# Kernel optimization log

Measured on AMD Instinct MI355X. Metric: run time of the kernel, lower is better.

Reference implementation:

```python
import jax, jax.numpy as jnp
import numpy as np

# einspline cubic B-spline basis matrix (4x4)
BASIS = jnp.array([[-1.0, 3.0, -3.0, 1.0],
                   [ 3.0, -6.0, 0.0, 4.0],
                   [-3.0, 3.0, 3.0, 1.0],
                   [ 1.0, 0.0, 0.0, 0.0]], dtype=jnp.float32) / 6.0


def _build_1d_system_matrix(M: int) -> jnp.ndarray:
    """(M+2, M+2) natural-boundary interpolating B-spline system matrix."""
    delta = 1.0 / (M - 1)
    dinv2 = (1.0 / delta) ** 2
    A = np.zeros((M + 2, M + 2), dtype=np.float32)
    A[0, 0] = dinv2; A[0, 1] = -2.0 * dinv2; A[0, 2] = dinv2
    i = np.arange(1, M + 1)
    A[i, i - 1] = 1.0 / 6.0
    A[i, i] = 2.0 / 3.0
    A[i, i + 1] = 1.0 / 6.0
    A[M + 1, M - 1] = dinv2; A[M + 1, M] = -2.0 * dinv2; A[M + 1, M + 1] = dinv2
    return jnp.asarray(A)


def find_coefs_2d(data: jnp.ndarray) -> jnp.ndarray:
    """data: (C, Mx, My) -> coefs: (C, Mx+2, My+2) via separable solves."""
    C, Mx, My = data.shape
    Ax = _build_1d_system_matrix(Mx)
    Ay = _build_1d_system_matrix(My)
    # solve along x for every (c, y)
    d = jnp.transpose(data, (0, 2, 1)).reshape(-1, Mx)          # (C*My, Mx)
    Bx = jnp.zeros((d.shape[0], Mx + 2), dtype=data.dtype).at[:, 1:Mx + 1].set(d)
    cx = jnp.linalg.solve(Ax, Bx.T).T                           # (C*My, Mx+2)
    cx = jnp.transpose(cx.reshape(C, My, Mx + 2), (0, 2, 1))    # (C, Mx+2, My)
    # solve along y for every (c, x)
    d2 = cx.reshape(-1, My)                                      # (C*(Mx+2), My)
    By = jnp.zeros((d2.shape[0], My + 2), dtype=data.dtype).at[:, 1:My + 1].set(d2)
    coefs = jnp.linalg.solve(Ay, By.T).T.reshape(C, Mx + 2, My + 2)
    return coefs


def _axis_index(un: jnp.ndarray, M: int):
    """Cell index + local fraction with out-of-range extrapolation handling."""
    i = jnp.floor(un).astype(jnp.int32)
    t = un - i.astype(un.dtype)
    low = un < 0
    i = jnp.where(low, 0, i)
    t = jnp.where(low, un, t)
    high = un >= M - 2
    i = jnp.where(high, M - 2, i)
    t = jnp.where(high, un - (M - 2), t)
    return i, t


def interpolate_grid_2d(coefs: jnp.ndarray, u: jnp.ndarray) -> jnp.ndarray:
    """coefs: (C, Mx+2, My+2); u: (B, 2) in [0,1]^2 -> (B, C)."""
    C, Mxp2, Myp2 = coefs.shape
    Mx, My = Mxp2 - 2, Myp2 - 2
    ux_norm = u[:, 0] * (Mx - 1)
    uy_norm = u[:, 1] * (My - 1)
    ix, tx = _axis_index(ux_norm, Mx)
    iy, ty = _axis_index(uy_norm, My)
    ones = jnp.ones_like(tx)
    tx_powers = jnp.stack([tx ** 3, tx ** 2, tx, ones], axis=0)  # (4, B)
    ty_powers = jnp.stack([ty ** 3, ty ** 2, ty, ones], axis=0)  # (4, B)
    basis_x = BASIS @ tx_powers                                   # (4, B)
    basis_y = BASIS @ ty_powers                                   # (4, B)
    offsets = jnp.arange(4, dtype=jnp.int32)
    ix_exp = ix[None, :] + offsets[:, None]                       # (4, B)
    iy_exp = iy[None, :] + offsets[:, None]                       # (4, B)
    # 4x4 neighborhood gather: (C, 4, 4, B)
    control_grid = coefs[:, ix_exp[:, None, :], iy_exp[None, :, :]]
    intermediate = jnp.einsum('cijb,ib->cjb', control_grid, basis_x)
    values = jnp.einsum('cjb,jb->cb', intermediate, basis_y)
    return values.T                                               # (B, C)


def setup_inputs() -> dict:
    key = jax.random.key(0)
    k_u, k_d = jax.random.split(key)
    u = jax.random.uniform(k_u, (2000000, 2), dtype=jnp.float32)
    data = jax.random.normal(k_d, (4, 64, 64), dtype=jnp.float32)
    return {"u": u, "data": data}


def reference(u, data):
    coefs = find_coefs_2d(data)
    return interpolate_grid_2d(coefs, u)
```

## Files before the change

kernel.cpp:

```cpp
#include <hip/hip_runtime.h>
#include <math.h>

#define MX 64
#define NC 4
#define NI 66
#define NINT 62

typedef _Float16 half4  __attribute__((ext_vector_type(4)));
typedef _Float16 half8  __attribute__((ext_vector_type(8)));
typedef _Float16 half2v __attribute__((ext_vector_type(2)));

struct TC { float m[NINT]; float inv[NINT]; };
constexpr TC make_tc() {
    TC tc{};
    double dp = 2.0/3.0;
    tc.m[0] = 0.0f;
    tc.inv[0] = (float)(1.0/dp);
    for (int j = 1; j < NINT; ++j) {
        double m = (1.0/6.0) / dp;
        tc.m[j] = (float)m;
        dp = 2.0/3.0 - m*(1.0/6.0);
        tc.inv[j] = (float)(1.0/dp);
    }
    return tc;
}
__constant__ constexpr TC g_tc = make_tc();

__device__ __forceinline__ float4 eval_pt(const char* __restrict__ taB,
                                          const char* __restrict__ tbB,
                                          float ux, float uy)
{
    const float unx = ux * 63.0f;
    const float uny = uy * 63.0f;

    int ix = (int)unx; ix = ix > 62 ? 62 : ix;
    int iy = (int)uny; iy = iy > 62 ? 62 : iy;
    const float tx = unx - (float)ix;
    const float ty = uny - (float)iy;

    const half2v t = __builtin_bit_cast(half2v, __builtin_amdgcn_cvt_pkrtz(tx, ty));
    const half2v c16  = half2v{(_Float16)(1.0f/6.0f), (_Float16)(1.0f/6.0f)};
    const half2v ch   = half2v{(_Float16)0.5f,  (_Float16)0.5f};
    const half2v cnh  = half2v{(_Float16)-0.5f, (_Float16)-0.5f};
    const half2v cn16 = half2v{(_Float16)(-1.0f/6.0f), (_Float16)(-1.0f/6.0f)};
    const half2v cn1  = half2v{(_Float16)-1.0f, (_Float16)-1.0f};
    const half2v c23  = half2v{(_Float16)(2.0f/3.0f), (_Float16)(2.0f/3.0f)};

    const half2v t2 = t*t;
    half2v b0 = (cn16*t + ch)*t;  b0 = (b0 + cnh)*t + c16;
    half2v b1 = (ch*t + cn1)*t2 + c23;
    half2v b2 = (cnh*t + ch)*t;   b2 = (b2 + ch)*t + c16;
    half2v b3 = c16*(t*t2);

    const half2v by0 = __builtin_shufflevector(b0, b0, 1, 1);
    const half2v by1 = __builtin_shufflevector(b1, b1, 1, 1);
    const half2v by2 = __builtin_shufflevector(b2, b2, 1, 1);
    const half2v by3 = __builtin_shufflevector(b3, b3, 1, 1);
    const half2v bx[4] = {
        __builtin_shufflevector(b0, b0, 0, 0),
        __builtin_shufflevector(b1, b1, 0, 0),
        __builtin_shufflevector(b2, b2, 0, 0),
        __builtin_shufflevector(b3, b3, 0, 0),
    };

    const int odd = iy & 1;
    const int ke  = iy >> 1;
    const char* base    = odd ? tbB : taB;
    const int   rstride = odd ? 512 : 528;
    const char* rp = base + ix*rstride + ke*16;

    half2v t01, t23;
    #pragma unroll
    for (int ar = 0; ar < 4; ++ar) {
        const half8 p0 = *(const half8*)(rp);
        const half8 p1 = *(const half8*)(rp + 16);
        rp += rstride;
        const half2v e0c01 = __builtin_shufflevector(p0, p0, 0, 1);
        const half2v e0c23 = __builtin_shufflevector(p0, p0, 2, 3);
        const half2v e1c01 = __builtin_shufflevector(p0, p0, 4, 5);
        const half2v e1c23 = __builtin_shufflevector(p0, p0, 6, 7);
        const half2v e2c01 = __builtin_shufflevector(p1, p1, 0, 1);
        const half2v e2c23 = __builtin_shufflevector(p1, p1, 2, 3);
        const half2v e3c01 = __builtin_shufflevector(p1, p1, 4, 5);
        const half2v e3c23 = __builtin_shufflevector(p1, p1, 6, 7);
        half2v a01 = e0c01*by0 + e1c01*by1 + e2c01*by2 + e3c01*by3;
        half2v a23 = e0c23*by0 + e1c23*by1 + e2c23*by2 + e3c23*by3;
        if (ar == 0) { t01 = a01*bx[0];        t23 = a23*bx[0]; }
        else         { t01 = a01*bx[ar] + t01; t23 = a23*bx[ar] + t23; }
    }
    return make_float4((float)t01.x, (float)t01.y, (float)t23.x, (float)t23.y);
}

__global__ __launch_bounds__(512, 4) void fused(const float2* __restrict__ uv,
                                                const float*  __restrict__ data,
                                                float4* __restrict__ out, int B)
{
    __shared__ __align__(16) half4 chS[NI*NI];
    __shared__ __align__(16) char  arenaB[2*NI*65*4];
    float (*cxS)[NI][65] = (float(*)[NI][65])arenaB;
    const int t = threadIdx.x;
    const float a = 1.0f/6.0f;

    #pragma unroll
    for (int c2 = 0; c2 < 2; ++c2) {
        if (t < 128) {
            const int cl = t >> 6, y = t & 63;
            const int c  = c2*2 + cl;
            const float* g = data + c*(MX*MX) + y;
            float w[NINT];
            const float d0 = g[0];
            #pragma unroll
            for (int j = 0; j < NINT; ++j) w[j] = g[(j+1)*MX];
            const float dM = g[63*MX];
            w[0]      -= a*d0;
            w[NINT-1] -= a*dM;
            #pragma unroll
            for (int j = 1; j < NINT; ++j) w[j] -= g_tc.m[j]*w[j-1];
            float x = w[NINT-1] * g_tc.inv[NINT-1];
            const float c63 = x;
            cxS[cl][63][y] = x;
            #pragma unroll
            for (int j = NINT-2; j >= 0; --j) {
                x = (w[j] - a*x) * g_tc.inv[j];
                cxS[cl][j+2][y] = x;
            }
            cxS[cl][0][y]  = 2.0f*d0 - x;
            cxS[cl][1][y]  = d0;
            cxS[cl][64][y] = dM;
            cxS[cl][65][y] = 2.0f*dM - c63;
        }
        __syncthreads();

        if (t < 2*NI) {
            const int cl = t / NI;
            const int i  = t - cl*NI;
            const int c  = c2*2 + cl;
            const float* g = &cxS[cl][i][0];
            _Float16* o = ((_Float16*)&chS[i*NI]) + c;

            float w[NINT];
            const float d0 = g[0];
            #pragma unroll
            for (int j = 0; j < NINT; ++j) w[j] = g[j+1];
            const float dM = g[63];
            w[0]      -= a*d0;
            w[NINT-1] -= a*dM;
            #pragma unroll
            for (int j = 1; j < NINT; ++j) w[j] -= g_tc.m[j]*w[j-1];
            float x = w[NINT-1] * g_tc.inv[NINT-1];
            const float c63 = x;
            o[63*NC] = (_Float16)x;
            #pragma unroll
            for (int j = NINT-2; j >= 0; --j) {
                x = (w[j] - a*x) * g_tc.inv[j];
                o[(j+2)*NC] = (_Float16)x;
            }
            o[0*NC]  = (_Float16)(2.0f*d0 - x);
            o[1*NC]  = (_Float16)d0;
            o[64*NC] = (_Float16)dM;
            o[65*NC] = (_Float16)(2.0f*dM - c63);
        }
        __syncthreads();
    }

    {
        half4* TB4 = (half4*)arenaB;
        for (int s = t; s < NI*32; s += 512) {
            const int i = s >> 5, k = s & 31;
            const half4* src = chS + i*NI + 2*k + 1;
            TB4[(i*32 + k)*2 + 0] = src[0];
            TB4[(i*32 + k)*2 + 1] = src[1];
        }
    }
    __syncthreads();

    const char* taB = (const char*)chS;
    const char* tbB = (const char*)arenaB;
    const int stride = gridDim.x * 512;
    for (int b = blockIdx.x*512 + t; b < B; b += stride) {
        const float2 uu = uv[b];
        out[b] = eval_pt(taB, tbB, uu.x, uu.y);
    }
}

extern "C" void kernel_launch(void* const* d_in, const int* in_sizes, int n_in,
                              void* d_out, int out_size, void* d_ws, size_t ws_size,
                              hipStream_t stream)
{
    const float* u    = (const float*)d_in[0];
    const float* data = (const float*)d_in[1];
    const int B  = in_sizes[0] / 2;

    fused<<<512, 512, 0, stream>>>((const float2*)u, data, (float4*)d_out, B);
}
```

Baseline: 82.96 us.

## Process two points per thread with 4-deep batched nontemporal loads and unified stride

Each thread now loads a float4 holding two points and processes four such loads per iteration, with all loads issued before evaluation to raise memory-level parallelism. Loads and stores use nontemporal hints. The odd-row table is padded to the same 528-byte stride as the even one, which removes the stride select, and launch bounds drop to 2 blocks per SM. This assumes B is even and changes LDS size and occupancy hints. Loads and stores are now strided by two points per lane, so per-instruction coalescing changes.

```diff
diff --git a/kernel.cpp b/kernel.cpp
--- a/kernel.cpp
+++ b/kernel.cpp
@@ -9,6 +9,7 @@
 typedef _Float16 half4  __attribute__((ext_vector_type(4)));
 typedef _Float16 half8  __attribute__((ext_vector_type(8)));
 typedef _Float16 half2v __attribute__((ext_vector_type(2)));
+typedef float    fx4    __attribute__((ext_vector_type(4)));
 
 struct TC { float m[NINT]; float inv[NINT]; };
 constexpr TC make_tc() {
@@ -26,9 +27,9 @@
 }
 __constant__ constexpr TC g_tc = make_tc();
 
-__device__ __forceinline__ float4 eval_pt(const char* __restrict__ taB,
-                                          const char* __restrict__ tbB,
-                                          float ux, float uy)
+__device__ __forceinline__ fx4 eval_pt(const char* __restrict__ taB,
+                                       const char* __restrict__ tbB,
+                                       float ux, float uy)
 {
     const float unx = ux * 63.0f;
     const float uny = uy * 63.0f;
@@ -65,16 +66,14 @@
 
     const int odd = iy & 1;
     const int ke  = iy >> 1;
-    const char* base    = odd ? tbB : taB;
-    const int   rstride = odd ? 512 : 528;
-    const char* rp = base + ix*rstride + ke*16;
+    const char* rp = (odd ? tbB : taB) + ix*528 + ke*16;
 
     half2v t01, t23;
     #pragma unroll
     for (int ar = 0; ar < 4; ++ar) {
         const half8 p0 = *(const half8*)(rp);
         const half8 p1 = *(const half8*)(rp + 16);
-        rp += rstride;
+        rp += 528;
         const half2v e0c01 = __builtin_shufflevector(p0, p0, 0, 1);
         const half2v e0c23 = __builtin_shufflevector(p0, p0, 2, 3);
         const half2v e1c01 = __builtin_shufflevector(p0, p0, 4, 5);
@@ -88,15 +87,15 @@
         if (ar == 0) { t01 = a01*bx[0];        t23 = a23*bx[0]; }
         else         { t01 = a01*bx[ar] + t01; t23 = a23*bx[ar] + t23; }
     }
-    return make_float4((float)t01.x, (float)t01.y, (float)t23.x, (float)t23.y);
-}
-
-__global__ __launch_bounds__(512, 4) void fused(const float2* __restrict__ uv,
-                                                const float*  __restrict__ data,
-                                                float4* __restrict__ out, int B)
+    return fx4{(float)t01.x, (float)t01.y, (float)t23.x, (float)t23.y};
+}
+
+__global__ __launch_bounds__(512, 2) void fused(const fx4* __restrict__ u2,
+                                                const float* __restrict__ data,
+                                                fx4* __restrict__ out, int NB)
 {
     __shared__ __align__(16) half4 chS[NI*NI];
-    __shared__ __align__(16) char  arenaB[2*NI*65*4];
+    __shared__ __align__(16) char  arenaB[NI*528];
     float (*cxS)[NI][65] = (float(*)[NI][65])arenaB;
     const int t = threadIdx.x;
     const float a = 1.0f/6.0f;
@@ -168,18 +167,34 @@
         for (int s = t; s < NI*32; s += 512) {
             const int i = s >> 5, k = s & 31;
             const half4* src = chS + i*NI + 2*k + 1;
-            TB4[(i*32 + k)*2 + 0] = src[0];
-            TB4[(i*32 + k)*2 + 1] = src[1];
+            TB4[i*66 + 2*k]     = src[0];
+            TB4[i*66 + 2*k + 1] = src[1];
         }
     }
     __syncthreads();
 
     const char* taB = (const char*)chS;
     const char* tbB = (const char*)arenaB;
-    const int stride = gridDim.x * 512;
-    for (int b = blockIdx.x*512 + t; b < B; b += stride) {
-        const float2 uu = uv[b];
-        out[b] = eval_pt(taB, tbB, uu.x, uu.y);
+    const int STRIDE = gridDim.x * 512;
+    for (int b0 = blockIdx.x*512 + t; b0 < NB; b0 += 4*STRIDE) {
+        fx4  ua[4];
+        bool ok[4];
+        #pragma unroll
+        for (int k = 0; k < 4; ++k) {
+            const int b = b0 + k*STRIDE;
+            ok[k] = (b < NB);
+            if (ok[k]) ua[k] = __builtin_nontemporal_load(&u2[b]);
+        }
+        #pragma unroll
+        for (int k = 0; k < 4; ++k) {
+            if (ok[k]) {
+                const int b = b0 + k*STRIDE;
+                const fx4 v0 = eval_pt(taB, tbB, ua[k].x, ua[k].y);
+                const fx4 v1 = eval_pt(taB, tbB, ua[k].z, ua[k].w);
+                __builtin_nontemporal_store(v0, &out[2*b]);
+                __builtin_nontemporal_store(v1, &out[2*b+1]);
+            }
+        }
     }
 }
 
@@ -190,6 +205,7 @@
     const float* u    = (const float*)d_in[0];
     const float* data = (const float*)d_in[1];
     const int B  = in_sizes[0] / 2;
-
-    fused<<<512, 512, 0, stream>>>((const float2*)u, data, (float4*)d_out, B);
-}
+    const int NB = B / 2;
+
+    fused<<<512, 512, 0, stream>>>((const fx4*)u, data, (fx4*)d_out, NB);
+}
```

Result: slower. 84.87 us (+2.3%).
